# Performance work log

Hardware: AMD Instinct MI355X
Metric: run time of the kernel (lower is better)

The kernel has to match this reference:

```python
import jax, jax.numpy as jnp
import numpy as np

N, D, C = 2097152, 64, 10  # samples, feature dim, classes


def setup_inputs() -> dict:
    key = jax.random.key(0)
    k1, k2, k3 = jax.random.split(key, 3)
    features = jax.random.normal(k1, (N, D), dtype=jnp.float32)
    sample_mean = jax.random.normal(k2, (C, D), dtype=jnp.float32)
    # precision is an inverse covariance -> symmetric PSD by construction
    A = jax.random.normal(k3, (D, D), dtype=jnp.float32) / np.float32(np.sqrt(D))
    precision = A @ A.T + 0.1 * jnp.eye(D, dtype=jnp.float32)
    alpha = jnp.ones((1,), dtype=jnp.float32)
    return {"features": features, "sample_mean": sample_mean,
            "precision": precision, "alpha": alpha}


def reference(features, sample_mean, precision, alpha):
    # gaussian_score[n, c] = -0.5 * (f_n - mu_c) P (f_n - mu_c)^T
    # Expanded (P symmetric): -0.5 * (f P f^T - 2 f P mu_c^T + mu_c P mu_c^T)
    fP = features @ precision                       # [N, D]
    qf = jnp.sum(fP * features, axis=-1)            # [N]  f P f^T (diag)
    muP = sample_mean @ precision                   # [C, D]
    qmu = jnp.sum(muP * sample_mean, axis=-1)       # [C]  mu P mu^T (diag)
    cross = features @ muP.T                        # [N, C]  f P mu_c^T
    gaussian_score = -0.5 * (qf[:, None] - 2.0 * cross + qmu[None, :])  # [N, C]
    # noise_gaussian_score: max over classes, scaled by layer alpha
    return alpha[0] * jnp.max(gaussian_score, axis=1)  # [N]
```

## Files before the change

### kernel.cpp

```cpp
#include <hip/hip_runtime.h>

#define NSAMP 2097152
#define DIM 64
#define NCLS 10
#define NT 5
#define TILES_PER_WAVE 8
#define WPB 4
#define SPB (WPB * 16 * TILES_PER_WAVE)

typedef __attribute__((ext_vector_type(8))) short short8;
typedef __attribute__((ext_vector_type(4))) float floatx4;

__device__ __forceinline__ unsigned bf16_rne_bits(float a) {
    unsigned u = __float_as_uint(a);
    return u + 0x7FFFu + ((u >> 16) & 1u);
}
__device__ __forceinline__ short f2bf(float a) { return (short)(bf16_rne_bits(a) >> 16); }
__device__ __forceinline__ float bf_hi_f(float a) {
    return __uint_as_float(bf16_rne_bits(a) & 0xFFFF0000u);
}
__device__ __forceinline__ float bf2f(short s) {
    return __uint_as_float(((unsigned)(unsigned short)s) << 16);
}
__device__ __forceinline__ unsigned pk2(float a, float b) {
    return (bf16_rne_bits(a) >> 16) | (bf16_rne_bits(b) & 0xFFFF0000u);
}

union S8 { unsigned u[4]; short8 v; };

__global__ __launch_bounds__(256) void precomp_kernel(
    const float* __restrict__ mu, const float* __restrict__ P,
    const float* __restrict__ alpha, void* __restrict__ ws)
{
    __shared__ float muP_s[NCLS * DIM];
    __shared__ float b_s[NCLS];
    short* mt_hi = (short*)ws;
    short* mt_lo = mt_hi + 80 * 64;
    float* bws   = (float*)(mt_hi + 2 * 80 * 64);

    const int t = threadIdx.x;
    for (int idx = t; idx < NCLS * DIM; idx += 256) {
        const int c = idx >> 6, j = idx & 63;
        float s = 0.f;
        #pragma unroll
        for (int i = 0; i < DIM; ++i) s += mu[c * DIM + i] * P[i * DIM + j];
        muP_s[idx] = s;
    }
    __syncthreads();
    if (t < NCLS) {
        float q = 0.f;
        #pragma unroll
        for (int j = 0; j < DIM; ++j) q += muP_s[t * DIM + j] * mu[t * DIM + j];
        b_s[t] = -0.5f * q;
    }
    __syncthreads();
    for (int idx = t; idx < 80 * 64; idx += 256) {
        const int n = idx >> 6, k = idx & 63;
        float v = 0.f;
        if (n < 64)       v = P[k * DIM + n];
        else if (n < 64 + NCLS) v = muP_s[(n - 64) * DIM + k];
        const short hi = f2bf(v);
        mt_hi[idx] = hi;
        mt_lo[idx] = f2bf(v - bf2f(hi));
    }
    if (t < 16) bws[t] = (t < NCLS) ? b_s[t] : -1e30f;
    if (t == 0) bws[16] = alpha[0];
}

__global__ __launch_bounds__(256) void mahal_kernel(
    const float* __restrict__ feat, const void* __restrict__ ws,
    float* __restrict__ out)
{
    const short* mt_hi = (const short*)ws;
    const short* mt_lo = mt_hi + 80 * 64;
    const float* bws   = (const float*)(mt_hi + 2 * 80 * 64);

    const int tid  = threadIdx.x;
    const int w    = tid >> 6;
    const int lane = tid & 63;
    const int ln   = lane & 15;
    const int q    = lane >> 4;

    __shared__ float fl[WPB][16 * 68];
    float* flw = &fl[w][0];

    short8 bh[NT][2], bl[NT][2];
    #pragma unroll
    for (int t = 0; t < NT; ++t)
        #pragma unroll
        for (int h = 0; h < 2; ++h) {
            const int off = (16 * t + ln) * 64 + h * 32 + q * 8;
            bh[t][h] = *(const short8*)(mt_hi + off);
            bl[t][h] = *(const short8*)(mt_lo + off);
        }
    const float bc    = bws[ln];
    const float alpha = bws[16];

    const long sbase0 = ((long)blockIdx.x * WPB + w) * (16 * TILES_PER_WAVE);

    #pragma unroll 1
    for (int it = 0; it < TILES_PER_WAVE; ++it) {
        const long sbase = sbase0 + (long)it * 16;

        const float* fr = feat + (sbase + ln) * DIM + q * 8;
        const float4 t0 = *(const float4*)(fr);
        const float4 t1 = *(const float4*)(fr + 4);
        const float4 t2 = *(const float4*)(fr + 32);
        const float4 t3 = *(const float4*)(fr + 36);

        float* fp = flw + ln * 68 + q * 8;
        *(float4*)(fp)      = t0;
        *(float4*)(fp + 4)  = t1;
        *(float4*)(fp + 32) = t2;
        *(float4*)(fp + 36) = t3;

        const float h0[8] = {t0.x, t0.y, t0.z, t0.w, t1.x, t1.y, t1.z, t1.w};
        const float h1[8] = {t2.x, t2.y, t2.z, t2.w, t3.x, t3.y, t3.z, t3.w};
        S8 ah0, ah1, al0, al1;
        #pragma unroll
        for (int i = 0; i < 4; ++i) {
            const float a0 = h0[2 * i], b0 = h0[2 * i + 1];
            const float a1 = h1[2 * i], b1 = h1[2 * i + 1];
            ah0.u[i] = pk2(a0, b0);
            ah1.u[i] = pk2(a1, b1);
            al0.u[i] = pk2(a0 - bf_hi_f(a0), b0 - bf_hi_f(b0));
            al1.u[i] = pk2(a1 - bf_hi_f(a1), b1 - bf_hi_f(b1));
        }
        const short8 A_h[2] = {ah0.v, ah1.v};
        const short8 A_l[2] = {al0.v, al1.v};

        floatx4 acc[NT];
        #pragma unroll
        for (int t = 0; t < NT; ++t) {
            floatx4 a = {0.f, 0.f, 0.f, 0.f};
            #pragma unroll
            for (int h = 0; h < 2; ++h) {
                a = __builtin_amdgcn_mfma_f32_16x16x32_bf16(A_h[h], bh[t][h], a, 0, 0, 0);
                a = __builtin_amdgcn_mfma_f32_16x16x32_bf16(A_h[h], bl[t][h], a, 0, 0, 0);
                a = __builtin_amdgcn_mfma_f32_16x16x32_bf16(A_l[h], bh[t][h], a, 0, 0, 0);
            }
            acc[t] = a;
        }

        float qf[4] = {0.f, 0.f, 0.f, 0.f};
        float sc[4];
        #pragma unroll
        for (int r = 0; r < 4; ++r) {
            const float* frow = flw + (q * 4 + r) * 68;
            #pragma unroll
            for (int t = 0; t < 4; ++t) qf[r] += acc[t][r] * frow[16 * t + ln];
            sc[r] = acc[4][r] + bc;
        }
        #pragma unroll
        for (int d = 1; d < 16; d <<= 1) {
            #pragma unroll
            for (int r = 0; r < 4; ++r) {
                qf[r] += __shfl_xor(qf[r], d);
                sc[r] = fmaxf(sc[r], __shfl_xor(sc[r], d));
            }
        }
        if (ln < 4) {
            const float qv = (ln == 0) ? qf[0] : (ln == 1) ? qf[1] : (ln == 2) ? qf[2] : qf[3];
            const float sv = (ln == 0) ? sc[0] : (ln == 1) ? sc[1] : (ln == 2) ? sc[2] : sc[3];
            out[sbase + q * 4 + ln] = alpha * (sv - 0.5f * qv);
        }
    }
}

extern "C" void kernel_launch(void* const* d_in, const int* in_sizes, int n_in,
                              void* d_out, int out_size, void* d_ws, size_t ws_size,
                              hipStream_t stream) {
    const float* features = (const float*)d_in[0];
    const float* mu       = (const float*)d_in[1];
    const float* P        = (const float*)d_in[2];
    const float* alpha    = (const float*)d_in[3];
    float* out = (float*)d_out;

    precomp_kernel<<<1, 256, 0, stream>>>(mu, P, alpha, d_ws);
    mahal_kernel<<<NSAMP / SPB, 256, 0, stream>>>(features, d_ws, out);
}
```

Baseline: 703.7 us.

## Prefetch next feature tile in registers and use hardware bf16 pack conversion

Loads the next 16-sample feature tile into registers while the current tile is processed, so global load latency overlaps MFMA and reduction work. Replaces software round-to-nearest bf16 packing with the v_cvt_pk_bf16_f32 instruction and derives the low part from the packed result. Moves precomputed matrices into device globals instead of the workspace pointer. Extra live registers for the prefetch buffer may lower occupancy.

Measured after the change: 701.7 us. No clear change (-0.3%).

```diff
diff --git a/kernel.cpp b/kernel.cpp
--- a/kernel.cpp
+++ b/kernel.cpp
@@ -11,32 +11,32 @@
 typedef __attribute__((ext_vector_type(8))) short short8;
 typedef __attribute__((ext_vector_type(4))) float floatx4;
 
+__device__ short g_mt_hi[80 * 64];
+__device__ short g_mt_lo[80 * 64];
+__device__ float g_b[20];
+
 __device__ __forceinline__ unsigned bf16_rne_bits(float a) {
     unsigned u = __float_as_uint(a);
     return u + 0x7FFFu + ((u >> 16) & 1u);
 }
 __device__ __forceinline__ short f2bf(float a) { return (short)(bf16_rne_bits(a) >> 16); }
-__device__ __forceinline__ float bf_hi_f(float a) {
-    return __uint_as_float(bf16_rne_bits(a) & 0xFFFF0000u);
-}
 __device__ __forceinline__ float bf2f(short s) {
     return __uint_as_float(((unsigned)(unsigned short)s) << 16);
 }
-__device__ __forceinline__ unsigned pk2(float a, float b) {
-    return (bf16_rne_bits(a) >> 16) | (bf16_rne_bits(b) & 0xFFFF0000u);
+__device__ __forceinline__ unsigned cvtpk_bf16(float a, float b) {
+    unsigned r;
+    asm("v_cvt_pk_bf16_f32 %0, %1, %2" : "=v"(r) : "v"(a), "v"(b));
+    return r;
 }
 
 union S8 { unsigned u[4]; short8 v; };
 
 __global__ __launch_bounds__(256) void precomp_kernel(
     const float* __restrict__ mu, const float* __restrict__ P,
-    const float* __restrict__ alpha, void* __restrict__ ws)
+    const float* __restrict__ alpha)
 {
     __shared__ float muP_s[NCLS * DIM];
     __shared__ float b_s[NCLS];
-    short* mt_hi = (short*)ws;
-    short* mt_lo = mt_hi + 80 * 64;
-    float* bws   = (float*)(mt_hi + 2 * 80 * 64);
 
     const int t = threadIdx.x;
     for (int idx = t; idx < NCLS * DIM; idx += 256) {
@@ -57,24 +57,19 @@
     for (int idx = t; idx < 80 * 64; idx += 256) {
         const int n = idx >> 6, k = idx & 63;
         float v = 0.f;
-        if (n < 64)       v = P[k * DIM + n];
+        if (n < 64)             v = P[k * DIM + n];
         else if (n < 64 + NCLS) v = muP_s[(n - 64) * DIM + k];
         const short hi = f2bf(v);
-        mt_hi[idx] = hi;
-        mt_lo[idx] = f2bf(v - bf2f(hi));
+        g_mt_hi[idx] = hi;
+        g_mt_lo[idx] = f2bf(v - bf2f(hi));
     }
-    if (t < 16) bws[t] = (t < NCLS) ? b_s[t] : -1e30f;
-    if (t == 0) bws[16] = alpha[0];
+    if (t < 16) g_b[t] = (t < NCLS) ? b_s[t] : -1e30f;
+    if (t == 0) g_b[16] = alpha[0];
 }
 
 __global__ __launch_bounds__(256) void mahal_kernel(
-    const float* __restrict__ feat, const void* __restrict__ ws,
-    float* __restrict__ out)
+    const float* __restrict__ feat, float* __restrict__ out)
 {
-    const short* mt_hi = (const short*)ws;
-    const short* mt_lo = mt_hi + 80 * 64;
-    const float* bws   = (const float*)(mt_hi + 2 * 80 * 64);
-
     const int tid  = threadIdx.x;
     const int w    = tid >> 6;
     const int lane = tid & 63;
@@ -90,23 +85,31 @@
         #pragma unroll
         for (int h = 0; h < 2; ++h) {
             const int off = (16 * t + ln) * 64 + h * 32 + q * 8;
-            bh[t][h] = *(const short8*)(mt_hi + off);
-            bl[t][h] = *(const short8*)(mt_lo + off);
+            bh[t][h] = *(const short8*)(g_mt_hi + off);
+            bl[t][h] = *(const short8*)(g_mt_lo + off);
         }
-    const float bc    = bws[ln];
-    const float alpha = bws[16];
+    const float bc    = g_b[ln];
+    const float alpha = g_b[16];
 
     const long sbase0 = ((long)blockIdx.x * WPB + w) * (16 * TILES_PER_WAVE);
+    const float* frbase = feat + (sbase0 + ln) * DIM + q * 8;
+
+    float4 t0 = *(const float4*)(frbase);
+    float4 t1 = *(const float4*)(frbase + 4);
+    float4 t2 = *(const float4*)(frbase + 32);
+    float4 t3 = *(const float4*)(frbase + 36);
 
     #pragma unroll 1
     for (int it = 0; it < TILES_PER_WAVE; ++it) {
-        const long sbase = sbase0 + (long)it * 16;
-
-        const float* fr = feat + (sbase + ln) * DIM + q * 8;
-        const float4 t0 = *(const float4*)(fr);
-        const float4 t1 = *(const float4*)(fr + 4);
-        const float4 t2 = *(const float4*)(fr + 32);
-        const float4 t3 = *(const float4*)(fr + 36);
+        float4 n0 = {0,0,0,0}, n1 = {0,0,0,0}, n2 = {0,0,0,0}, n3 = {0,0,0,0};
+        const bool more = (it + 1 < TILES_PER_WAVE);
+        if (more) {
+            const float* fr = frbase + (size_t)(it + 1) * (16 * DIM);
+            n0 = *(const float4*)(fr);
+            n1 = *(const float4*)(fr + 4);
+            n2 = *(const float4*)(fr + 32);
+            n3 = *(const float4*)(fr + 36);
+        }
 
         float* fp = flw + ln * 68 + q * 8;
         *(float4*)(fp)      = t0;
@@ -121,10 +124,14 @@
         for (int i = 0; i < 4; ++i) {
             const float a0 = h0[2 * i], b0 = h0[2 * i + 1];
             const float a1 = h1[2 * i], b1 = h1[2 * i + 1];
-            ah0.u[i] = pk2(a0, b0);
-            ah1.u[i] = pk2(a1, b1);
-            al0.u[i] = pk2(a0 - bf_hi_f(a0), b0 - bf_hi_f(b0));
-            al1.u[i] = pk2(a1 - bf_hi_f(a1), b1 - bf_hi_f(b1));
+            const unsigned rh0 = cvtpk_bf16(a0, b0);
+            const unsigned rh1 = cvtpk_bf16(a1, b1);
+            ah0.u[i] = rh0;
+            ah1.u[i] = rh1;
+            al0.u[i] = cvtpk_bf16(a0 - __uint_as_float(rh0 << 16),
+                                  b0 - __uint_as_float(rh0 & 0xFFFF0000u));
+            al1.u[i] = cvtpk_bf16(a1 - __uint_as_float(rh1 << 16),
+                                  b1 - __uint_as_float(rh1 & 0xFFFF0000u));
         }
         const short8 A_h[2] = {ah0.v, ah1.v};
         const short8 A_l[2] = {al0.v, al1.v};
@@ -162,8 +169,10 @@
         if (ln < 4) {
             const float qv = (ln == 0) ? qf[0] : (ln == 1) ? qf[1] : (ln == 2) ? qf[2] : qf[3];
             const float sv = (ln == 0) ? sc[0] : (ln == 1) ? sc[1] : (ln == 2) ? sc[2] : sc[3];
-            out[sbase + q * 4 + ln] = alpha * (sv - 0.5f * qv);
+            out[sbase0 + (size_t)it * 16 + q * 4 + ln] = alpha * (sv - 0.5f * qv);
         }
+
+        if (more) { t0 = n0; t1 = n1; t2 = n2; t3 = n3; }
     }
 }
 
@@ -174,8 +183,8 @@
     const float* mu       = (const float*)d_in[1];
     const float* P        = (const float*)d_in[2];
     const float* alpha    = (const float*)d_in[3];
-    float* out = (float*)d_out;
+    (void)d_ws; (void)ws_size; (void)in_sizes; (void)n_in; (void)out_size;
 
-    precomp_kernel<<<1, 256, 0, stream>>>(mu, P, alpha, d_ws);
-    mahal_kernel<<<NSAMP / SPB, 256, 0, stream>>>(features, d_ws, out);
+    precomp_kernel<<<1, 256, 0, stream>>>(mu, P, alpha);
+    mahal_kernel<<<NSAMP / SPB, 256, 0, stream>>>(features, (float*)d_out);
 }
```
